# Performance work log

Measured on AMD Instinct MI355X. Metric: run time of the kernel, lower is better.

The kernel has to match this reference:

```python
import jax, jax.numpy as jnp
import numpy as np

VOCAB, NUM_CLASSES, E, H = 50257, 20, 64, 64
B, T = 128, 2048


def setup_inputs() -> dict:
    key = jax.random.key(0)
    ks = jax.random.split(key, 16)
    s_ih = 1.0 / np.sqrt(H)
    u = lambda k, shape: jax.random.uniform(k, shape, jnp.float32, -s_ih, s_ih)
    return {
        'tokens': jax.random.randint(ks[0], (B, T), 0, VOCAB),
        'emb': jax.random.normal(ks[1], (VOCAB, E), jnp.float32),
        # forward-direction GRU params (PyTorch layout: [3H, *], gate order r,z,n)
        'wih_f': u(ks[2], (3 * H, E)), 'whh_f': u(ks[3], (3 * H, H)),
        'bih_f': u(ks[4], (3 * H,)), 'bhh_f': u(ks[5], (3 * H,)),
        # backward-direction GRU params
        'wih_b': u(ks[6], (3 * H, E)), 'whh_b': u(ks[7], (3 * H, H)),
        'bih_b': u(ks[8], (3 * H,)), 'bhh_b': u(ks[9], (3 * H,)),
        # classifier: Linear(4H -> H), GELU, Linear(H -> C)
        'w1': u(ks[10], (H, 4 * H)), 'b1': u(ks[11], (H,)),
        'w2': u(ks[12], (NUM_CLASSES, H)), 'b2': u(ks[13], (NUM_CLASSES,)),
    }


def _gru_dir(x, wih, whh, bih, bhh):
    # x: [B, T, E] -> outputs [B, T, H]; PyTorch GRU gate math, gates (r, z, n)
    xg = jnp.einsum('bte,ge->tbg', x, wih) + bih  # precompute input projections [T,B,3H]
    h0 = jnp.zeros((x.shape[0], H), x.dtype)

    def step(h, xg_t):
        hg = h @ whh.T + bhh
        xr, xz, xn = jnp.split(xg_t, 3, axis=-1)
        hr, hz, hn = jnp.split(hg, 3, axis=-1)
        r = jax.nn.sigmoid(xr + hr)
        z = jax.nn.sigmoid(xz + hz)
        n = jnp.tanh(xn + r * hn)
        h_new = (1.0 - z) * n + z * h
        return h_new, h_new

    _, hs = jax.lax.scan(step, h0, xg)  # hs: [T, B, H]
    return hs.transpose(1, 0, 2)


def reference(tokens, emb, wih_f, whh_f, bih_f, bhh_f,
              wih_b, whh_b, bih_b, bhh_b, w1, b1, w2, b2):
    x = emb[tokens]  # [B, T, E]
    h_fwd = _gru_dir(x, wih_f, whh_f, bih_f, bhh_f)
    h_bwd = _gru_dir(x[:, ::-1], wih_b, whh_b, bih_b, bhh_b)[:, ::-1]
    encoded = jnp.concatenate([h_fwd, h_bwd], axis=-1)  # [B, T, 2H]
    feats = jnp.concatenate([encoded.mean(axis=1), encoded.max(axis=1)], axis=-1)  # [B, 4H]
    hid = jax.nn.gelu(feats @ w1.T + b1, approximate=False)
    return hid @ w2.T + b2  # [B, C]
```

## Files before the change

kernel.cpp:

```cpp
#include <hip/hip_runtime.h>
#include <hip/hip_bf16.h>
#include <math.h>

#define VOCAB 50257
#define NCLS 20
#define EDIM 64
#define HDIM 64
#define BATCH 128
#define TLEN 2048

typedef float v2f __attribute__((ext_vector_type(2)));

__device__ float g_P[(size_t)2 * VOCAB * 192];
__device__ float g_feats[BATCH * 256];

__device__ __forceinline__ float fast_rcp(float x) { return __builtin_amdgcn_rcpf(x); }

__device__ __forceinline__ float fsigmoid(float x) {
    return fast_rcp(1.f + __expf(-x));
}
__device__ __forceinline__ float ftanh(float x) {
    float e = __expf(2.f * x);
    return 1.f - 2.f * fast_rcp(e + 1.f);
}

__global__ __launch_bounds__(384) void precompute_P(
    const float* __restrict__ emb,
    const float* __restrict__ wih_f, const float* __restrict__ bih_f,
    const float* __restrict__ wih_b, const float* __restrict__ bih_b)
{
    const int t = threadIdx.x;
    const int dir = t / 192;
    const int g = t % 192;
    const float* wih = dir ? wih_b : wih_f;
    const float* bih = dir ? bih_b : bih_f;

    float w[64];
#pragma unroll
    for (int e = 0; e < 64; e += 4) {
        float4 v = *(const float4*)(wih + (size_t)g * 64 + e);
        w[e] = v.x; w[e + 1] = v.y; w[e + 2] = v.z; w[e + 3] = v.w;
    }
    const float bias = bih[g];
    float* Pd = g_P + (size_t)dir * VOCAB * 192;

    for (int v = blockIdx.x * 2; v < VOCAB; v += gridDim.x * 2) {
        const int v1ok = (v + 1 < VOCAB);
        const float4* e0 = (const float4*)(emb + (size_t)v * 64);
        const float4* e1 = (const float4*)(emb + (size_t)(v1ok ? v + 1 : v) * 64);
        float a0 = bias, a1 = bias;
#pragma unroll
        for (int e4 = 0; e4 < 16; e4++) {
            float4 x = e0[e4];
            float4 y = e1[e4];
            a0 = fmaf(x.x, w[4 * e4 + 0], a0);
            a1 = fmaf(y.x, w[4 * e4 + 0], a1);
            a0 = fmaf(x.y, w[4 * e4 + 1], a0);
            a1 = fmaf(y.y, w[4 * e4 + 1], a1);
            a0 = fmaf(x.z, w[4 * e4 + 2], a0);
            a1 = fmaf(y.z, w[4 * e4 + 2], a1);
            a0 = fmaf(x.w, w[4 * e4 + 3], a0);
            a1 = fmaf(y.w, w[4 * e4 + 3], a1);
        }
        Pd[(size_t)v * 192 + g] = a0;
        if (v1ok) Pd[(size_t)(v + 1) * 192 + g] = a1;
    }
}

__global__ __launch_bounds__(64, 1) __attribute__((amdgpu_waves_per_eu(1, 1)))
void gru_seq(
    const int* __restrict__ tokens,
    const float* __restrict__ whh_f, const float* __restrict__ bhh_f,
    const float* __restrict__ whh_b, const float* __restrict__ bhh_b)
{
    const int lane = threadIdx.x;
    const int blk = blockIdx.x;
    const int b = blk >> 1;
    const int dir = blk & 1;
    const float* whh = dir ? whh_b : whh_f;
    const float* bhh = dir ? bhh_b : bhh_f;
    const float* Pd = g_P + (size_t)dir * VOCAB * 192;

    __shared__ __align__(16) float h_lds[64];
    __shared__ __align__(16) int tok_lds[TLEN];

    {
        const int4* src = (const int4*)(tokens + (size_t)b * TLEN);
        int4* dst = (int4*)tok_lds;
        for (int t = lane; t < TLEN / 4; t += 64) dst[t] = src[t];
    }

    v2f wr[32], wz[32], wn[32];
    {
        const float* pr = whh + (size_t)(0 + lane) * 64;
        const float* pz = whh + (size_t)(64 + lane) * 64;
        const float* pn = whh + (size_t)(128 + lane) * 64;
#pragma unroll
        for (int k = 0; k < 16; k++) {
            float4 a = *(const float4*)(pr + 4 * k);
            wr[2 * k] = (v2f){a.x, a.y}; wr[2 * k + 1] = (v2f){a.z, a.w};
            float4 c = *(const float4*)(pz + 4 * k);
            wz[2 * k] = (v2f){c.x, c.y}; wz[2 * k + 1] = (v2f){c.z, c.w};
            float4 d = *(const float4*)(pn + 4 * k);
            wn[2 * k] = (v2f){d.x, d.y}; wn[2 * k + 1] = (v2f){d.z, d.w};
        }
    }
    const float br = bhh[lane], bz = bhh[64 + lane], bn = bhh[128 + lane];

    h_lds[lane] = 0.f;
    float h = 0.f, sum = 0.f, mx = -INFINITY;

    auto tok_at = [&](int s) -> int {
        int ss = s < TLEN ? s : TLEN - 1;
        return tok_lds[dir ? (TLEN - 1 - ss) : ss];
    };

    float xr0, xz0, xn0, xr1, xz1, xn1, xr2, xz2, xn2, xr3, xz3, xn3;

#define GRU_PRE(SL, D) do {                                                        \
        const float* rd_ = Pd + (size_t)tok_at(D) * 192;                           \
        asm volatile("global_load_dword %0, %1, off" : "=v"(xr##SL) : "v"(rd_ + lane));       \
        asm volatile("global_load_dword %0, %1, off" : "=v"(xz##SL) : "v"(rd_ + 64 + lane));  \
        asm volatile("global_load_dword %0, %1, off" : "=v"(xn##SL) : "v"(rd_ + 128 + lane)); \
    } while (0)

    GRU_PRE(0, 0); GRU_PRE(1, 1); GRU_PRE(2, 2); GRU_PRE(3, 3);

#define GRU_STEP(SL, SB) do {                                                      \
        const int tN_ = tok_at((SB) + 4);                                          \
        v2f ar0 = {0.f, 0.f}, ar1 = {0.f, 0.f};                                    \
        v2f az0 = {0.f, 0.f}, az1 = {0.f, 0.f};                                    \
        v2f an0 = {0.f, 0.f}, an1 = {0.f, 0.f};                                    \
        _Pragma("unroll")                                                          \
        for (int k = 0; k < 16; k++) {                                             \
            float4 h4 = *(const float4*)(h_lds + 4 * k);                           \
            v2f h01 = {h4.x, h4.y}, h23 = {h4.z, h4.w};                            \
            ar0 = __builtin_elementwise_fma(h01, wr[2 * k], ar0);                  \
            az0 = __builtin_elementwise_fma(h01, wz[2 * k], az0);                  \
            an0 = __builtin_elementwise_fma(h01, wn[2 * k], an0);                  \
            ar1 = __builtin_elementwise_fma(h23, wr[2 * k + 1], ar1);              \
            az1 = __builtin_elementwise_fma(h23, wz[2 * k + 1], az1);              \
            an1 = __builtin_elementwise_fma(h23, wn[2 * k + 1], an1);              \
        }                                                                          \
        float hr = (ar0.x + ar0.y) + (ar1.x + ar1.y);                              \
        float hz = (az0.x + az0.y) + (az1.x + az1.y);                              \
        float hn = (an0.x + an0.y) + (an1.x + an1.y);                              \
          \
        asm volatile("s_waitcnt vmcnt(9)"                                          \
                     : "+v"(xr##SL), "+v"(xz##SL), "+v"(xn##SL));                  \
        float r_ = fsigmoid(xr##SL + hr + br);                                     \
        float z_ = fsigmoid(xz##SL + hz + bz);                                     \
        float n_ = ftanh(xn##SL + r_ * (hn + bn));                                 \
        h = fmaf(z_, h - n_, n_);                               \
        sum += h;                                                                  \
        mx = fmaxf(mx, h);                                                         \
        h_lds[lane] = h;              \
        const float* rp_ = Pd + (size_t)tN_ * 192;                                 \
        asm volatile("global_load_dword %0, %1, off" : "=v"(xr##SL) : "v"(rp_ + lane));       \
        asm volatile("global_load_dword %0, %1, off" : "=v"(xz##SL) : "v"(rp_ + 64 + lane));  \
        asm volatile("global_load_dword %0, %1, off" : "=v"(xn##SL) : "v"(rp_ + 128 + lane)); \
    } while (0)

    for (int s = 0; s < TLEN; s += 4) {
        GRU_STEP(0, s + 0);
        GRU_STEP(1, s + 1);
        GRU_STEP(2, s + 2);
        GRU_STEP(3, s + 3);
    }
    asm volatile("s_waitcnt vmcnt(0)" ::: "memory");

    g_feats[b * 256 + dir * 64 + lane] = sum * (1.f / TLEN);
    g_feats[b * 256 + 128 + dir * 64 + lane] = mx;
#undef GRU_PRE
#undef GRU_STEP
}

__global__ __launch_bounds__(64) void classifier(
    const float* __restrict__ w1, const float* __restrict__ b1,
    const float* __restrict__ w2, const float* __restrict__ b2,
    float* __restrict__ out)
{
    const int b = blockIdx.x;
    const int i = threadIdx.x;
    __shared__ float f[256];
    __shared__ float hid[64];
    for (int c = i; c < 256; c += 64) f[c] = g_feats[b * 256 + c];
    __syncthreads();

    float acc = b1[i];
    const float* wrow = w1 + (size_t)i * 256;
#pragma unroll 16
    for (int c = 0; c < 256; c++) acc = fmaf(f[c], wrow[c], acc);
    hid[i] = acc * 0.5f * (1.f + erff(acc * 0.70710678118654752f));
    __syncthreads();

    if (i < NCLS) {
        float o = b2[i];
        const float* w2r = w2 + (size_t)i * 64;
#pragma unroll
        for (int j = 0; j < 64; j++) o = fmaf(hid[j], w2r[j], o);
        out[b * NCLS + i] = o;
    }
}

extern "C" void kernel_launch(void* const* d_in, const int* in_sizes, int n_in,
                              void* d_out, int out_size, void* d_ws, size_t ws_size,
                              hipStream_t stream) {
    const int*   tokens = (const int*)  d_in[0];
    const float* emb    = (const float*)d_in[1];
    const float* wih_f  = (const float*)d_in[2];
    const float* whh_f  = (const float*)d_in[3];
    const float* bih_f  = (const float*)d_in[4];
    const float* bhh_f  = (const float*)d_in[5];
    const float* wih_b  = (const float*)d_in[6];
    const float* whh_b  = (const float*)d_in[7];
    const float* bih_b  = (const float*)d_in[8];
    const float* bhh_b  = (const float*)d_in[9];
    const float* w1     = (const float*)d_in[10];
    const float* b1     = (const float*)d_in[11];
    const float* w2     = (const float*)d_in[12];
    const float* b2     = (const float*)d_in[13];
    float* out = (float*)d_out;

    precompute_P<<<4096, 384, 0, stream>>>(emb, wih_f, bih_f, wih_b, bih_b);
    gru_seq<<<2 * BATCH, 64, 0, stream>>>(tokens, whh_f, bhh_f, whh_b, bhh_b);
    classifier<<<BATCH, 64, 0, stream>>>(w1, b1, w2, b2, out);
}
```

Measured before the change: 950.1 us.

## Split GRU recurrence across three waves, one per gate, with LDS exchange

Each sequence/direction block now uses three wavefronts, each holding one gate's recurrent weight rows and computing that gate's 64-wide matvec. The r and z waves write their sigmoid outputs to LDS; after a barrier the n wave computes the candidate, updates h and the running mean/max, and publishes h for the next step. This shortens each wave's serial FMA chain per timestep by a factor of three and cuts register pressure. In exchange it adds two block barriers and LDS round trips per step on the critical path.

```diff
diff --git a/kernel.cpp b/kernel.cpp
--- a/kernel.cpp
+++ b/kernel.cpp
@@ -67,98 +67,95 @@
     }
 }
 
-__global__ __launch_bounds__(64, 1) __attribute__((amdgpu_waves_per_eu(1, 1)))
-void gru_seq(
+__global__ __launch_bounds__(192, 1) void gru_seq(
     const int* __restrict__ tokens,
     const float* __restrict__ whh_f, const float* __restrict__ bhh_f,
     const float* __restrict__ whh_b, const float* __restrict__ bhh_b)
 {
-    const int lane = threadIdx.x;
+    const int tid = threadIdx.x;
+    const int wid = tid >> 6;
+    const int lane = tid & 63;
     const int blk = blockIdx.x;
     const int b = blk >> 1;
     const int dir = blk & 1;
     const float* whh = dir ? whh_b : whh_f;
     const float* bhh = dir ? bhh_b : bhh_f;
-    const float* Pd = g_P + (size_t)dir * VOCAB * 192;
+    const float* Pd = g_P + (size_t)dir * VOCAB * 192 + wid * 64 + lane;
 
     __shared__ __align__(16) float h_lds[64];
+    __shared__ float r_lds[64];
+    __shared__ float z_lds[64];
     __shared__ __align__(16) int tok_lds[TLEN];
 
     {
         const int4* src = (const int4*)(tokens + (size_t)b * TLEN);
         int4* dst = (int4*)tok_lds;
-        for (int t = lane; t < TLEN / 4; t += 64) dst[t] = src[t];
-    }
-
-    v2f wr[32], wz[32], wn[32];
+        for (int t = tid; t < TLEN / 4; t += 192) dst[t] = src[t];
+    }
+
+    v2f w[32];
     {
-        const float* pr = whh + (size_t)(0 + lane) * 64;
-        const float* pz = whh + (size_t)(64 + lane) * 64;
-        const float* pn = whh + (size_t)(128 + lane) * 64;
+        const float* p = whh + (size_t)(wid * 64 + lane) * 64;
 #pragma unroll
         for (int k = 0; k < 16; k++) {
-            float4 a = *(const float4*)(pr + 4 * k);
-            wr[2 * k] = (v2f){a.x, a.y}; wr[2 * k + 1] = (v2f){a.z, a.w};
-            float4 c = *(const float4*)(pz + 4 * k);
-            wz[2 * k] = (v2f){c.x, c.y}; wz[2 * k + 1] = (v2f){c.z, c.w};
-            float4 d = *(const float4*)(pn + 4 * k);
-            wn[2 * k] = (v2f){d.x, d.y}; wn[2 * k + 1] = (v2f){d.z, d.w};
+            float4 a = *(const float4*)(p + 4 * k);
+            w[2 * k] = (v2f){a.x, a.y};
+            w[2 * k + 1] = (v2f){a.z, a.w};
         }
     }
-    const float br = bhh[lane], bz = bhh[64 + lane], bn = bhh[128 + lane];
-
-    h_lds[lane] = 0.f;
+    const float bias = bhh[wid * 64 + lane];
+
+    if (wid == 2) h_lds[lane] = 0.f;
     float h = 0.f, sum = 0.f, mx = -INFINITY;
+    __syncthreads();
 
     auto tok_at = [&](int s) -> int {
         int ss = s < TLEN ? s : TLEN - 1;
         return tok_lds[dir ? (TLEN - 1 - ss) : ss];
     };
 
-    float xr0, xz0, xn0, xr1, xz1, xn1, xr2, xz2, xn2, xr3, xz3, xn3;
-
-#define GRU_PRE(SL, D) do {                                                        \
-        const float* rd_ = Pd + (size_t)tok_at(D) * 192;                           \
-        asm volatile("global_load_dword %0, %1, off" : "=v"(xr##SL) : "v"(rd_ + lane));       \
-        asm volatile("global_load_dword %0, %1, off" : "=v"(xz##SL) : "v"(rd_ + 64 + lane));  \
-        asm volatile("global_load_dword %0, %1, off" : "=v"(xn##SL) : "v"(rd_ + 128 + lane)); \
-    } while (0)
-
+    float x0, x1, x2, x3;
+#define GRU_PRE(SL, D) \
+    asm volatile("global_load_dword %0, %1, off" : "=v"(x##SL) : "v"(Pd + (size_t)tok_at(D) * 192))
     GRU_PRE(0, 0); GRU_PRE(1, 1); GRU_PRE(2, 2); GRU_PRE(3, 3);
 
 #define GRU_STEP(SL, SB) do {                                                      \
-        const int tN_ = tok_at((SB) + 4);                                          \
-        v2f ar0 = {0.f, 0.f}, ar1 = {0.f, 0.f};                                    \
-        v2f az0 = {0.f, 0.f}, az1 = {0.f, 0.f};                                    \
-        v2f an0 = {0.f, 0.f}, an1 = {0.f, 0.f};                                    \
+        const int tN_ = tok_at((SB) + 4);    \
+        v2f a0 = {0.f, 0.f}, a1 = {0.f, 0.f};                                      \
         _Pragma("unroll")                                                          \
         for (int k = 0; k < 16; k++) {                                             \
             float4 h4 = *(const float4*)(h_lds + 4 * k);                           \
             v2f h01 = {h4.x, h4.y}, h23 = {h4.z, h4.w};                            \
-            ar0 = __builtin_elementwise_fma(h01, wr[2 * k], ar0);                  \
-            az0 = __builtin_elementwise_fma(h01, wz[2 * k], az0);                  \
-            an0 = __builtin_elementwise_fma(h01, wn[2 * k], an0);                  \
-            ar1 = __builtin_elementwise_fma(h23, wr[2 * k + 1], ar1);              \
-            az1 = __builtin_elementwise_fma(h23, wz[2 * k + 1], az1);              \
-            an1 = __builtin_elementwise_fma(h23, wn[2 * k + 1], an1);              \
+            a0 = __builtin_elementwise_fma(h01, w[2 * k], a0);                     \
+            a1 = __builtin_elementwise_fma(h23, w[2 * k + 1], a1);                 \
         }                                                                          \
-        float hr = (ar0.x + ar0.y) + (ar1.x + ar1.y);                              \
-        float hz = (az0.x + az0.y) + (az1.x + az1.y);                              \
-        float hn = (an0.x + an0.y) + (an1.x + an1.y);                              \
-          \
-        asm volatile("s_waitcnt vmcnt(9)"                                          \
-                     : "+v"(xr##SL), "+v"(xz##SL), "+v"(xn##SL));                  \
-        float r_ = fsigmoid(xr##SL + hr + br);                                     \
-        float z_ = fsigmoid(xz##SL + hz + bz);                                     \
-        float n_ = ftanh(xn##SL + r_ * (hn + bn));                                 \
-        h = fmaf(z_, h - n_, n_);                               \
-        sum += h;                                                                  \
-        mx = fmaxf(mx, h);                                                         \
-        h_lds[lane] = h;              \
-        const float* rp_ = Pd + (size_t)tN_ * 192;                                 \
-        asm volatile("global_load_dword %0, %1, off" : "=v"(xr##SL) : "v"(rp_ + lane));       \
-        asm volatile("global_load_dword %0, %1, off" : "=v"(xz##SL) : "v"(rp_ + 64 + lane));  \
-        asm volatile("global_load_dword %0, %1, off" : "=v"(xn##SL) : "v"(rp_ + 128 + lane)); \
+        float hg = (a0.x + a0.y) + (a1.x + a1.y);                                  \
+        if (wid != 2) {                                                            \
+                    \
+            asm volatile("s_waitcnt vmcnt(3)" : "+v"(x##SL));                      \
+            float g_ = fsigmoid(x##SL + hg + bias);                                \
+            (wid == 0 ? r_lds : z_lds)[lane] = g_;                                 \
+            asm volatile("global_load_dword %0, %1, off"                           \
+                         : "=v"(x##SL) : "v"(Pd + (size_t)tN_ * 192));             \
+        }                                                                          \
+        asm volatile("s_waitcnt lgkmcnt(0)" ::: "memory");   \
+        __builtin_amdgcn_s_barrier();                          \
+        __builtin_amdgcn_sched_barrier(0);                                         \
+        if (wid == 2) {                                                            \
+            asm volatile("s_waitcnt vmcnt(3)" : "+v"(x##SL));                      \
+            float r_ = r_lds[lane];                                                \
+            float z_ = z_lds[lane];                                                \
+            float n_ = ftanh(x##SL + r_ * (hg + bias));                            \
+            h = fmaf(z_, h - n_, n_);                           \
+            sum += h;                                                              \
+            mx = fmaxf(mx, h);                                                     \
+            h_lds[lane] = h;                                                       \
+            asm volatile("global_load_dword %0, %1, off"                           \
+                         : "=v"(x##SL) : "v"(Pd + (size_t)tN_ * 192));             \
+        }                                                                          \
+        asm volatile("s_waitcnt lgkmcnt(0)" ::: "memory");    \
+        __builtin_amdgcn_s_barrier();                              \
+        __builtin_amdgcn_sched_barrier(0);                                         \
     } while (0)
 
     for (int s = 0; s < TLEN; s += 4) {
@@ -169,8 +166,10 @@
     }
     asm volatile("s_waitcnt vmcnt(0)" ::: "memory");
 
-    g_feats[b * 256 + dir * 64 + lane] = sum * (1.f / TLEN);
-    g_feats[b * 256 + 128 + dir * 64 + lane] = mx;
+    if (wid == 2) {
+        g_feats[b * 256 + dir * 64 + lane] = sum * (1.f / TLEN);
+        g_feats[b * 256 + 128 + dir * 64 + lane] = mx;
+    }
 #undef GRU_PRE
 #undef GRU_STEP
 }
@@ -223,6 +222,6 @@
     float* out = (float*)d_out;
 
     precompute_P<<<4096, 384, 0, stream>>>(emb, wih_f, bih_f, wih_b, bih_b);
-    gru_seq<<<2 * BATCH, 64, 0, stream>>>(tokens, whh_f, bhh_f, whh_b, bhh_b);
+    gru_seq<<<2 * BATCH, 192, 0, stream>>>(tokens, whh_f, bhh_f, whh_b, bhh_b);
     classifier<<<BATCH, 64, 0, stream>>>(w1, b1, w2, b2, out);
 }
```

Result: slower. 980.1 us (+3.2%).
